# Kernel tuning notes

Hardware: AMD Instinct MI355X
Metric: run time of the kernel (lower is better)

## Reference

```python
import jax, jax.numpy as jnp
import numpy as np

QUERY_DIM = 1024
CONTEXT_DIM = 1024
HEADS = 8
DIM_HEAD = 64
INNER = HEADS * DIM_HEAD  # 512
SCALE = DIM_HEAD ** -0.5


def setup_inputs() -> dict:
    key = jax.random.key(0)
    ks = jax.random.split(key, 7)
    B, N, M = 2, 2048, 2048
    x = jax.random.normal(ks[0], (B, N, QUERY_DIM), dtype=jnp.float32)
    context = jax.random.normal(ks[1], (B, M, CONTEXT_DIM), dtype=jnp.float32)
    # nn.Linear weights (stored as [out, in] in torch; we use [in, out] here)
    Wq = jax.random.normal(ks[2], (QUERY_DIM, INNER), dtype=jnp.float32) * (QUERY_DIM ** -0.5)
    Wk = jax.random.normal(ks[3], (CONTEXT_DIM, INNER), dtype=jnp.float32) * (CONTEXT_DIM ** -0.5)
    Wv = jax.random.normal(ks[4], (CONTEXT_DIM, INNER), dtype=jnp.float32) * (CONTEXT_DIM ** -0.5)
    Wo = jax.random.normal(ks[5], (INNER, QUERY_DIM), dtype=jnp.float32) * (INNER ** -0.5)
    bo = jax.random.normal(ks[6], (QUERY_DIM,), dtype=jnp.float32) * 0.01
    return {"x": x, "context": context, "Wq": Wq, "Wk": Wk, "Wv": Wv, "Wo": Wo, "bo": bo}


def reference(x, context, Wq, Wk, Wv, Wo, bo):
    B, N, _ = x.shape
    M = context.shape[1]
    # projections (no bias, matching nn.Linear(bias=False))
    q = (x @ Wq).reshape(B, N, HEADS, DIM_HEAD)          # b i h d
    k = (context @ Wk).reshape(B, M, HEADS, DIM_HEAD)    # b j h d
    v = (context @ Wv).reshape(B, M, HEADS, DIM_HEAD)    # b j h d
    # scores in fp32 (ATTN_PRECISION=='fp32' path)
    sim = jnp.einsum('bihd,bjhd->bhij', q.astype(jnp.float32), k.astype(jnp.float32)) * SCALE
    attn = jax.nn.softmax(sim, axis=-1).astype(v.dtype)  # b h i j
    out = jnp.einsum('bhij,bjhd->bihd', attn, v).reshape(B, N, INNER)
    return out @ Wo + bo  # dropout p=0.0 is identity
```

## Files before the change

kernel.cpp:

```cpp
#include <hip/hip_runtime.h>
#include <math.h>

typedef __bf16 bf16_t;
typedef __bf16 bf16x8 __attribute__((ext_vector_type(8)));
typedef __bf16 bf16x4 __attribute__((ext_vector_type(4)));
typedef float  f32x4  __attribute__((ext_vector_type(4)));

#define MFMA16(a, b, c) __builtin_amdgcn_mfma_f32_16x16x32_bf16((a), (b), (c), 0, 0, 0)

#define INNER   512
#define DHEAD   64
#define QSCALE  0.18033688f

__device__ __forceinline__ void g2l(const bf16_t* g, bf16_t* l) {
  __builtin_amdgcn_global_load_lds(
      (const __attribute__((address_space(1))) unsigned int*)g,
      (__attribute__((address_space(3))) unsigned int*)l, 16, 0, 0);
}

__global__ __launch_bounds__(256) void pre_w_k(const float* __restrict__ Wq,
                                               const float* __restrict__ Wk,
                                               const float* __restrict__ Wv,
                                               const float* __restrict__ Wo,
                                               bf16_t* __restrict__ WqT,
                                               bf16_t* __restrict__ WkT,
                                               bf16_t* __restrict__ WvT,
                                               bf16_t* __restrict__ WoT) {
  __shared__ float tile[64][65];
  int t = blockIdx.x;
  int z = t >> 7, bid = t & 127;
  const float* W; bf16_t* WT; int K, N;
  if (z == 0)      { W = Wq; WT = WqT; K = 1024; N = 512; }
  else if (z == 1) { W = Wk; WT = WkT; K = 1024; N = 512; }
  else if (z == 2) { W = Wv; WT = WvT; K = 1024; N = 512; }
  else             { W = Wo; WT = WoT; K = 512;  N = 1024; }
  int tK = K >> 6;
  int kt = bid % tK, nt = bid / tK;
  int k0 = kt << 6, n0 = nt << 6;
  for (int idx = threadIdx.x; idx < 4096; idx += 256) {
    int r = idx >> 6, c = idx & 63;
    tile[r][c] = W[(size_t)(k0 + r) * N + n0 + c];
  }
  __syncthreads();
  for (int idx = threadIdx.x; idx < 4096; idx += 256) {
    int r = idx >> 6, c = idx & 63;
    WT[(size_t)(n0 + r) * K + k0 + c] = (bf16_t)tile[c][r];
  }
}

template<int BM, bool AF32>
__device__ __forceinline__ void gemm_core(const void* __restrict__ Ap,
                                          const bf16_t* __restrict__ Bt,
                                          int K, int N, int row0, int n0,
                                          int mode, float scale,
                                          bf16_t* __restrict__ Cb,
                                          float* __restrict__ Cf,
                                          const float* __restrict__ bias) {
  constexpr int MI = BM / 32;
  __shared__ bf16_t As[2 * BM * 64];
  __shared__ bf16_t Bs[2 * 128 * 64];
  const int tid = threadIdx.x;
  const int w = tid >> 6, lane = tid & 63, quad = lane >> 4, l16 = lane & 15;

  const int sr8  = lane >> 3;
  const int slog = ((lane & 7) ^ sr8) << 3;
  const float*  gaF = nullptr;
  const bf16_t* gaB = nullptr;
  {
    size_t aoff = (size_t)(row0 + w * (BM / 4) + sr8) * K + slog;
    if constexpr (AF32) gaF = (const float*)Ap + aoff;
    else                gaB = (const bf16_t*)Ap + aoff;
  }
  const bf16_t* gb = Bt + (size_t)(n0 + w * 32 + sr8) * K + slog;
  bf16_t* lA = As + w * (BM / 4) * 64;
  bf16_t* lB = Bs + w * 2048;

  f32x4 acc[MI][4];
#pragma unroll
  for (int i = 0; i < MI; ++i)
#pragma unroll
    for (int j = 0; j < 4; ++j) acc[i][j] = f32x4{0.f, 0.f, 0.f, 0.f};

  const int mrow = (w & 1) * (BM / 2), ncol = (w >> 1) << 6;
  const int KT = K >> 6;

  if constexpr (AF32) {
#pragma unroll
    for (int p = 0; p < MI; ++p) {
      const float* s = gaF + (size_t)(p * 8) * K;
      f32x4 f0 = *(const f32x4*)s;
      f32x4 f1 = *(const f32x4*)(s + 4);
      bf16x8 h;
#pragma unroll
      for (int e = 0; e < 4; ++e) { h[e] = (bf16_t)f0[e]; h[4 + e] = (bf16_t)f1[e]; }
      *(bf16x8*)&lA[p * 512 + lane * 8] = h;
    }
  } else {
#pragma unroll
    for (int p = 0; p < MI; ++p)
      g2l(gaB + (size_t)(p * 8) * K, lA + p * 512);
  }
#pragma unroll
  for (int p = 0; p < 4; ++p)
    g2l(gb + (size_t)(p * 8) * K, lB + p * 512);

  for (int kc = 0; kc < KT; ++kc) {
    const int curA = (kc & 1) * (BM * 64), nxtA = ((kc + 1) & 1) * (BM * 64);
    const int curB = (kc & 1) * 8192,      nxtB = ((kc + 1) & 1) * 8192;
    __syncthreads();
    f32x4 fpre[2 * MI];
    const bool pf = (kc + 1 < KT);
    if (pf) {
      const int k0 = (kc + 1) * 64;
#pragma unroll
      for (int p = 0; p < 4; ++p)
        g2l(gb + (size_t)(p * 8) * K + k0, lB + nxtB + p * 512);
      if constexpr (AF32) {
#pragma unroll
        for (int p = 0; p < MI; ++p) {
          const float* s = gaF + (size_t)(p * 8) * K + k0;
          fpre[2 * p]     = *(const f32x4*)s;
          fpre[2 * p + 1] = *(const f32x4*)(s + 4);
        }
      } else {
#pragma unroll
        for (int p = 0; p < MI; ++p)
          g2l(gaB + (size_t)(p * 8) * K + k0, lA + nxtA + p * 512);
      }
    }
#pragma unroll
    for (int ks = 0; ks < 2; ++ks) {
      const int phys = ((ks * 4 + quad) ^ (l16 & 7)) << 3;
      bf16x8 af[MI], bfr[4];
#pragma unroll
      for (int i = 0; i < MI; ++i)
        af[i] = *(const bf16x8*)&As[curA + (mrow + i * 16 + l16) * 64 + phys];
#pragma unroll
      for (int j = 0; j < 4; ++j)
        bfr[j] = *(const bf16x8*)&Bs[curB + (ncol + j * 16 + l16) * 64 + phys];
#pragma unroll
      for (int i = 0; i < MI; ++i)
#pragma unroll
        for (int j = 0; j < 4; ++j)
          acc[i][j] = MFMA16(af[i], bfr[j], acc[i][j]);
    }
    if (pf) {
      if constexpr (AF32) {
#pragma unroll
        for (int p = 0; p < MI; ++p) {
          bf16x8 h;
#pragma unroll
          for (int e = 0; e < 4; ++e) {
            h[e]     = (bf16_t)fpre[2 * p][e];
            h[4 + e] = (bf16_t)fpre[2 * p + 1][e];
          }
          *(bf16x8*)&lA[nxtA + p * 512 + lane * 8] = h;
        }
      }
    }
  }

#pragma unroll
  for (int i = 0; i < MI; ++i) {
    int row = row0 + mrow + i * 16 + quad * 4;
#pragma unroll
    for (int j = 0; j < 4; ++j) {
      int col = n0 + ncol + j * 16 + l16;
      if (mode == 2) {
        int bb = row >> 11, key = row & 2047;
        int hh = col >> 6,  d   = col & 63;
        bf16x4 v = { (bf16_t)acc[i][j][0], (bf16_t)acc[i][j][1],
                     (bf16_t)acc[i][j][2], (bf16_t)acc[i][j][3] };
        *(bf16x4*)&Cb[((size_t)((bb * 8 + hh) * 64 + d)) * 2048 + key] = v;
      } else {
#pragma unroll
        for (int r = 0; r < 4; ++r) {
          if (mode == 1) Cf[(size_t)(row + r) * N + col] = acc[i][j][r] + bias[col];
          else           Cb[(size_t)(row + r) * N + col] = (bf16_t)(acc[i][j][r] * scale);
        }
      }
    }
  }
}

__global__ __launch_bounds__(256, 2) void gemm_qkv_k(const float* __restrict__ x,
                                                     const float* __restrict__ ctx,
                                                     const bf16_t* __restrict__ WqT,
                                                     const bf16_t* __restrict__ WkT,
                                                     const bf16_t* __restrict__ WvT,
                                                     bf16_t* __restrict__ Qb,
                                                     bf16_t* __restrict__ Kb,
                                                     bf16_t* __restrict__ Vt) {
  int z = blockIdx.z;
  const float* A   = (z == 0) ? x   : ctx;
  const bf16_t* Bt = (z == 0) ? WqT : (z == 1) ? WkT : WvT;
  bf16_t* C        = (z == 0) ? Qb  : (z == 1) ? Kb  : Vt;
  int mode         = (z == 2) ? 2 : 0;
  float scale      = (z == 0) ? QSCALE : 1.0f;
  gemm_core<128, true>(A, Bt, 1024, 512, blockIdx.y * 128, blockIdx.x * 128,
                       mode, scale, C, nullptr, nullptr);
}

__global__ __launch_bounds__(256, 2) void gemm_out_k(const bf16_t* __restrict__ AO,
                                                     const bf16_t* __restrict__ WoT,
                                                     const float* __restrict__ bo,
                                                     float* __restrict__ out) {
  gemm_core<64, false>(AO, WoT, 512, 1024, blockIdx.y * 64, blockIdx.x * 128,
                       1, 1.0f, nullptr, out, bo);
}

__global__ __launch_bounds__(256, 2) void attn_k(const bf16_t* __restrict__ Qb,
                                                 const bf16_t* __restrict__ Kb,
                                                 const bf16_t* __restrict__ Vt,
                                                 bf16_t* __restrict__ AO) {
  const int tid = threadIdx.x;
  const int w = tid >> 6, lane = tid & 63, quad = lane >> 4, l16 = lane & 15;
  const int qt = blockIdx.x;
  const int bh = blockIdx.y;
  const int b = bh >> 3, h = bh & 7;

  __shared__ bf16_t Ks[2 * 128 * 64];
  __shared__ bf16_t Vs[64 * 128];
  __shared__ bf16_t Ps[64 * 136];

  const int qrow = b * 2048 + qt * 64 + w * 16 + l16;
  const bf16_t* qptr = Qb + (size_t)qrow * INNER + h * DHEAD;
  bf16x8 bq[2];
  bq[0] = *(const bf16x8*)(qptr + quad * 8);
  bq[1] = *(const bf16x8*)(qptr + 32 + quad * 8);

  f32x4 o[4];
#pragma unroll
  for (int dt = 0; dt < 4; ++dt) o[dt] = f32x4{0.f, 0.f, 0.f, 0.f};
  float m_s = -__builtin_inff(), l_s = 0.f;

  const bf16_t* kbase  = Kb + ((size_t)b * 2048) * INNER + h * DHEAD;
  const bf16_t* vtbase = Vt + ((size_t)bh * 64) * 2048;

  const int krow = lane >> 3;
  const int kcol = ((lane & 7) ^ (lane >> 3)) << 3;
  const int vrow = lane >> 4;

#pragma unroll
  for (int p = 0; p < 4; ++p)
    g2l(kbase + (size_t)(w * 32 + p * 8 + krow) * INNER + kcol,
        &Ks[w * 2048 + p * 512]);

  for (int kt = 0; kt < 16; ++kt) {
    const int cur = (kt & 1) * 8192, nxt = ((kt + 1) & 1) * 8192;
    __syncthreads();
    if (kt < 16 - 1) {
#pragma unroll
      for (int p = 0; p < 4; ++p)
        g2l(kbase + (size_t)((kt + 1) * 128 + w * 32 + p * 8 + krow) * INNER + kcol,
            &Ks[nxt + w * 2048 + p * 512]);
    }
#pragma unroll
    for (int p = 0; p < 4; ++p) {
      int vlog = ((lane & 15) ^ ((p * 4 + vrow) & 15)) << 3;
      g2l(vtbase + (size_t)(w * 16 + p * 4 + vrow) * 2048 + kt * 128 + vlog,
          &Vs[w * 2048 + p * 512]);
    }

    f32x4 s[8];
#pragma unroll
    for (int jt = 0; jt < 8; ++jt) s[jt] = f32x4{0.f, 0.f, 0.f, 0.f};
#pragma unroll
    for (int jt = 0; jt < 8; ++jt) {
#pragma unroll
      for (int ks = 0; ks < 2; ++ks) {
        int phys = ((ks * 4 + quad) ^ (l16 & 7)) << 3;
        bf16x8 ak = *(const bf16x8*)&Ks[cur + (jt * 16 + l16) * 64 + phys];
        s[jt] = MFMA16(ak, bq[ks], s[jt]);
      }
    }

    float mx = -__builtin_inff();
#pragma unroll
    for (int jt = 0; jt < 8; ++jt) {
      float a = fmaxf(fmaxf(s[jt][0], s[jt][1]), fmaxf(s[jt][2], s[jt][3]));
      mx = fmaxf(mx, a);
    }
    mx = fmaxf(mx, __shfl_xor(mx, 16, 64));
    mx = fmaxf(mx, __shfl_xor(mx, 32, 64));
    float mnew = fmaxf(m_s, mx);
    float alpha = __builtin_amdgcn_exp2f(m_s - mnew);
    float rs = 0.f;
#pragma unroll
    for (int jt = 0; jt < 8; ++jt) {
#pragma unroll
      for (int r = 0; r < 4; ++r) {
        float p = __builtin_amdgcn_exp2f(s[jt][r] - mnew);
        s[jt][r] = p;
        rs += p;
      }
    }
    rs += __shfl_xor(rs, 16, 64);
    rs += __shfl_xor(rs, 32, 64);
    l_s = l_s * alpha + rs;
    m_s = mnew;
#pragma unroll
    for (int dt = 0; dt < 4; ++dt) o[dt] *= alpha;

#pragma unroll
    for (int jt = 0; jt < 8; ++jt) {
      bf16x4 pk = { (bf16_t)s[jt][0], (bf16_t)s[jt][1],
                    (bf16_t)s[jt][2], (bf16_t)s[jt][3] };
      *(bf16x4*)&Ps[(w * 16 + l16) * 136 + jt * 16 + quad * 4] = pk;
    }

    __syncthreads();

#pragma unroll
    for (int kc = 0; kc < 4; ++kc) {
      bf16x8 bp = *(const bf16x8*)&Ps[(w * 16 + l16) * 136 + kc * 32 + quad * 8];
#pragma unroll
      for (int dt = 0; dt < 4; ++dt) {
        int phys = ((kc * 4 + quad) ^ l16) << 3;
        bf16x8 av = *(const bf16x8*)&Vs[(dt * 16 + l16) * 128 + phys];
        o[dt] = MFMA16(av, bp, o[dt]);
      }
    }
  }

  float inv = 1.0f / l_s;
#pragma unroll
  for (int dt = 0; dt < 4; ++dt) {
    bf16x4 ov = { (bf16_t)(o[dt][0] * inv), (bf16_t)(o[dt][1] * inv),
                  (bf16_t)(o[dt][2] * inv), (bf16_t)(o[dt][3] * inv) };
    *(bf16x4*)&Ps[(w * 16 + l16) * 136 + dt * 16 + quad * 4] = ov;
  }
  __syncthreads();
  {
    int sr = tid >> 2, sc = (tid & 3) << 4;
    int4 r0 = *(const int4*)&Ps[sr * 136 + sc];
    int4 r1 = *(const int4*)&Ps[sr * 136 + sc + 8];
    bf16_t* aout = AO + ((size_t)(b * 2048 + qt * 64 + sr)) * INNER + h * DHEAD + sc;
    *(int4*)aout       = r0;
    *(int4*)(aout + 8) = r1;
  }
}

extern "C" void kernel_launch(void* const* d_in, const int* in_sizes, int n_in,
                              void* d_out, int out_size, void* d_ws, size_t ws_size,
                              hipStream_t stream) {
  const float* x   = (const float*)d_in[0];
  const float* ctx = (const float*)d_in[1];
  const float* Wq  = (const float*)d_in[2];
  const float* Wk  = (const float*)d_in[3];
  const float* Wv  = (const float*)d_in[4];
  const float* Wo  = (const float*)d_in[5];
  const float* bo  = (const float*)d_in[6];
  float* out = (float*)d_out;

  char* ws = (char*)d_ws;
  const size_t MB = 1048576;
  bf16_t* WqT = (bf16_t*)(ws + 0 * MB);
  bf16_t* WkT = (bf16_t*)(ws + 1 * MB);
  bf16_t* WvT = (bf16_t*)(ws + 2 * MB);
  bf16_t* WoT = (bf16_t*)(ws + 3 * MB);
  bf16_t* Qb  = (bf16_t*)(ws + 4 * MB);
  bf16_t* Kb  = (bf16_t*)(ws + 8 * MB);
  bf16_t* Vt  = (bf16_t*)(ws + 12 * MB);
  bf16_t* AO  = (bf16_t*)(ws + 16 * MB);

  pre_w_k<<<512, 256, 0, stream>>>(Wq, Wk, Wv, Wo, WqT, WkT, WvT, WoT);
  gemm_qkv_k<<<dim3(4, 32, 3), 256, 0, stream>>>(x, ctx, WqT, WkT, WvT, Qb, Kb, Vt);
  attn_k<<<dim3(32, 16), 256, 0, stream>>>(Qb, Kb, Vt, AO);
  gemm_out_k<<<dim3(8, 64), 256, 0, stream>>>(AO, WoT, bo, out);
}
```

Baseline: 169.5 us.

## Fuse all four stages into one persistent kernel with grid barriers

Replaces the four separate launches (weight transpose, QKV projection, attention, output projection) with a single 512-block persistent kernel. The stages are separated by atomic-counter grid barriers and share one statically sized shared-memory buffer. The V projection now uses 64-row tiles so that all 512 blocks get work in the QKV stage. This is meant to remove launch gaps and per-kernel ramp overhead. In exchange it adds a memset, barrier spin costs, and the risk of deadlock if the 512 blocks cannot all be resident at once.

```diff
diff --git a/kernel.cpp b/kernel.cpp
--- a/kernel.cpp
+++ b/kernel.cpp
@@ -11,6 +11,7 @@
 #define INNER   512
 #define DHEAD   64
 #define QSCALE  0.18033688f
+#define NBLK    512u
 
 __device__ __forceinline__ void g2l(const bf16_t* g, bf16_t* l) {
   __builtin_amdgcn_global_load_lds(
@@ -18,16 +19,31 @@
       (__attribute__((address_space(3))) unsigned int*)l, 16, 0, 0);
 }
 
-__global__ __launch_bounds__(256) void pre_w_k(const float* __restrict__ Wq,
-                                               const float* __restrict__ Wk,
-                                               const float* __restrict__ Wv,
-                                               const float* __restrict__ Wo,
-                                               bf16_t* __restrict__ WqT,
-                                               bf16_t* __restrict__ WkT,
-                                               bf16_t* __restrict__ WvT,
-                                               bf16_t* __restrict__ WoT) {
-  __shared__ float tile[64][65];
-  int t = blockIdx.x;
+__device__ __forceinline__ void gridbar(unsigned int* bar, unsigned int phase) {
+  __threadfence();
+  __syncthreads();
+  if (threadIdx.x == 0) {
+    __hip_atomic_fetch_add(bar, 1u, __ATOMIC_ACQ_REL, __HIP_MEMORY_SCOPE_AGENT);
+    const unsigned int goal = phase * NBLK;
+    while (__hip_atomic_load(bar, __ATOMIC_ACQUIRE,
+                             __HIP_MEMORY_SCOPE_AGENT) < goal) {
+      __builtin_amdgcn_s_sleep(2);
+    }
+  }
+  __syncthreads();
+  __threadfence();
+}
+
+__device__ __forceinline__ void pre_w_stage(int t, bf16_t* sm,
+                                            const float* __restrict__ Wq,
+                                            const float* __restrict__ Wk,
+                                            const float* __restrict__ Wv,
+                                            const float* __restrict__ Wo,
+                                            bf16_t* __restrict__ WqT,
+                                            bf16_t* __restrict__ WkT,
+                                            bf16_t* __restrict__ WvT,
+                                            bf16_t* __restrict__ WoT) {
+  float* tile = (float*)sm;
   int z = t >> 7, bid = t & 127;
   const float* W; bf16_t* WT; int K, N;
   if (z == 0)      { W = Wq; WT = WqT; K = 1024; N = 512; }
@@ -39,17 +55,18 @@
   int k0 = kt << 6, n0 = nt << 6;
   for (int idx = threadIdx.x; idx < 4096; idx += 256) {
     int r = idx >> 6, c = idx & 63;
-    tile[r][c] = W[(size_t)(k0 + r) * N + n0 + c];
+    tile[r * 65 + c] = W[(size_t)(k0 + r) * N + n0 + c];
   }
   __syncthreads();
   for (int idx = threadIdx.x; idx < 4096; idx += 256) {
     int r = idx >> 6, c = idx & 63;
-    WT[(size_t)(n0 + r) * K + k0 + c] = (bf16_t)tile[c][r];
+    WT[(size_t)(n0 + r) * K + k0 + c] = (bf16_t)tile[c * 65 + r];
   }
 }
 
 template<int BM, bool AF32>
-__device__ __forceinline__ void gemm_core(const void* __restrict__ Ap,
+__device__ __forceinline__ void gemm_core(bf16_t* sm,
+                                          const void* __restrict__ Ap,
                                           const bf16_t* __restrict__ Bt,
                                           int K, int N, int row0, int n0,
                                           int mode, float scale,
@@ -57,8 +74,8 @@
                                           float* __restrict__ Cf,
                                           const float* __restrict__ bias) {
   constexpr int MI = BM / 32;
-  __shared__ bf16_t As[2 * BM * 64];
-  __shared__ bf16_t Bs[2 * 128 * 64];
+  bf16_t* As = sm;
+  bf16_t* Bs = sm + 2 * BM * 64;
   const int tid = threadIdx.x;
   const int w = tid >> 6, lane = tid & 63, quad = lane >> 4, l16 = lane & 15;
 
@@ -183,45 +200,20 @@
   }
 }
 
-__global__ __launch_bounds__(256, 2) void gemm_qkv_k(const float* __restrict__ x,
-                                                     const float* __restrict__ ctx,
-                                                     const bf16_t* __restrict__ WqT,
-                                                     const bf16_t* __restrict__ WkT,
-                                                     const bf16_t* __restrict__ WvT,
-                                                     bf16_t* __restrict__ Qb,
-                                                     bf16_t* __restrict__ Kb,
-                                                     bf16_t* __restrict__ Vt) {
-  int z = blockIdx.z;
-  const float* A   = (z == 0) ? x   : ctx;
-  const bf16_t* Bt = (z == 0) ? WqT : (z == 1) ? WkT : WvT;
-  bf16_t* C        = (z == 0) ? Qb  : (z == 1) ? Kb  : Vt;
-  int mode         = (z == 2) ? 2 : 0;
-  float scale      = (z == 0) ? QSCALE : 1.0f;
-  gemm_core<128, true>(A, Bt, 1024, 512, blockIdx.y * 128, blockIdx.x * 128,
-                       mode, scale, C, nullptr, nullptr);
-}
-
-__global__ __launch_bounds__(256, 2) void gemm_out_k(const bf16_t* __restrict__ AO,
-                                                     const bf16_t* __restrict__ WoT,
-                                                     const float* __restrict__ bo,
-                                                     float* __restrict__ out) {
-  gemm_core<64, false>(AO, WoT, 512, 1024, blockIdx.y * 64, blockIdx.x * 128,
-                       1, 1.0f, nullptr, out, bo);
-}
-
-__global__ __launch_bounds__(256, 2) void attn_k(const bf16_t* __restrict__ Qb,
-                                                 const bf16_t* __restrict__ Kb,
-                                                 const bf16_t* __restrict__ Vt,
-                                                 bf16_t* __restrict__ AO) {
+__device__ __forceinline__ void attn_stage(int bid, bf16_t* sm,
+                                           const bf16_t* __restrict__ Qb,
+                                           const bf16_t* __restrict__ Kb,
+                                           const bf16_t* __restrict__ Vt,
+                                           bf16_t* __restrict__ AO) {
+  bf16_t* Ks = sm;
+  bf16_t* Vs = sm + 16384;
+  bf16_t* Ps = sm + 24576;
+
   const int tid = threadIdx.x;
   const int w = tid >> 6, lane = tid & 63, quad = lane >> 4, l16 = lane & 15;
-  const int qt = blockIdx.x;
-  const int bh = blockIdx.y;
+  const int qt = bid & 31;
+  const int bh = bid >> 5;
   const int b = bh >> 3, h = bh & 7;
-
-  __shared__ bf16_t Ks[2 * 128 * 64];
-  __shared__ bf16_t Vs[64 * 128];
-  __shared__ bf16_t Ps[64 * 136];
 
   const int qrow = b * 2048 + qt * 64 + w * 16 + l16;
   const bf16_t* qptr = Qb + (size_t)qrow * INNER + h * DHEAD;
@@ -339,6 +331,43 @@
     *(int4*)aout       = r0;
     *(int4*)(aout + 8) = r1;
   }
+}
+
+__global__ __launch_bounds__(256, 2) void fused_k(
+    const float* __restrict__ x,   const float* __restrict__ ctx,
+    const float* __restrict__ Wq,  const float* __restrict__ Wk,
+    const float* __restrict__ Wv,  const float* __restrict__ Wo,
+    const float* __restrict__ bo,
+    bf16_t* __restrict__ WqT, bf16_t* __restrict__ WkT,
+    bf16_t* __restrict__ WvT, bf16_t* __restrict__ WoT,
+    bf16_t* __restrict__ Qb,  bf16_t* __restrict__ Kb,
+    bf16_t* __restrict__ Vt,  bf16_t* __restrict__ AO,
+    float* __restrict__ out,  unsigned int* bar) {
+  __shared__ __align__(16) bf16_t smem[33280];
+  const int bid = blockIdx.x;
+
+  pre_w_stage(bid, smem, Wq, Wk, Wv, Wo, WqT, WkT, WvT, WoT);
+  gridbar(bar, 1u);
+
+  if (bid < 128) {
+    gemm_core<128, true>(smem, x, WqT, 1024, 512, (bid >> 2) * 128, (bid & 3) * 128,
+                         0, QSCALE, Qb, nullptr, nullptr);
+  } else if (bid < 256) {
+    int t = bid - 128;
+    gemm_core<128, true>(smem, ctx, WkT, 1024, 512, (t >> 2) * 128, (t & 3) * 128,
+                         0, 1.0f, Kb, nullptr, nullptr);
+  } else {
+    int t = bid - 256;
+    gemm_core<64, true>(smem, ctx, WvT, 1024, 512, (t >> 2) * 64, (t & 3) * 128,
+                        2, 1.0f, Vt, nullptr, nullptr);
+  }
+  gridbar(bar, 2u);
+
+  attn_stage(bid, smem, Qb, Kb, Vt, AO);
+  gridbar(bar, 3u);
+
+  gemm_core<64, false>(smem, AO, WoT, 512, 1024, (bid >> 3) * 64, (bid & 7) * 128,
+                       1, 1.0f, nullptr, out, bo);
 }
 
 extern "C" void kernel_launch(void* const* d_in, const int* in_sizes, int n_in,
@@ -363,9 +392,11 @@
   bf16_t* Kb  = (bf16_t*)(ws + 8 * MB);
   bf16_t* Vt  = (bf16_t*)(ws + 12 * MB);
   bf16_t* AO  = (bf16_t*)(ws + 16 * MB);
-
-  pre_w_k<<<512, 256, 0, stream>>>(Wq, Wk, Wv, Wo, WqT, WkT, WvT, WoT);
-  gemm_qkv_k<<<dim3(4, 32, 3), 256, 0, stream>>>(x, ctx, WqT, WkT, WvT, Qb, Kb, Vt);
-  attn_k<<<dim3(32, 16), 256, 0, stream>>>(Qb, Kb, Vt, AO);
-  gemm_out_k<<<dim3(8, 64), 256, 0, stream>>>(AO, WoT, bo, out);
-}
+  unsigned int* bar = (unsigned int*)(ws + 20 * MB);
+
+  hipMemsetAsync((void*)bar, 0, 64, stream);
+
+  fused_k<<<dim3(512), dim3(256), 0, stream>>>(
+      x, ctx, Wq, Wk, Wv, Wo, bo,
+      WqT, WkT, WvT, WoT, Qb, Kb, Vt, AO, out, bar);
+}
```

Result: slower. 584.4 us (+244.8%).
